# Kernel optimization log

Hardware: AMD Instinct MI355X
Metric: run time of the kernel (lower is better)

Reference implementation:

```python
import jax, jax.numpy as jnp
import numpy as np

TOP_K = 2
NEG_INF = -1e30


def setup_inputs() -> dict:
    key = jax.random.key(0)
    ks = jax.random.split(key, 9)
    S, B, D, H, E, O = 2, 2048, 1024, 2048, 8, 1024
    return {
        "xs": jax.random.normal(ks[0], (S, B, D), jnp.float32),
        "Wg": jax.random.normal(ks[1], (D, E), jnp.float32),
        "b": jax.random.normal(ks[2], (E,), jnp.float32),
        "fc1_w": jax.random.normal(ks[3], (E, H, D), jnp.float32) * 0.02,
        "fc1_b": jax.random.normal(ks[4], (E, H), jnp.float32) * 0.02,
        "fc2_w": jax.random.normal(ks[5], (E, H, H), jnp.float32) * 0.02,
        "fc2_b": jax.random.normal(ks[6], (E, H), jnp.float32) * 0.02,
        "final_w": jax.random.normal(ks[7], (O, H), jnp.float32) * 0.02,
        "final_b": jax.random.normal(ks[8], (O,), jnp.float32) * 0.02,
    }


def reference(xs, Wg, b, fc1_w, fc1_b, fc2_w, fc2_b, final_w, final_b):
    # xs: [S, B, D] stacked x_list
    S = xs.shape[0]
    # gate logits H: [S, B, E]
    Hg = jnp.einsum('sbd,de->sbe', xs, Wg) + b
    expert_probs = jax.nn.softmax(Hg, axis=-1)  # per-view full softmax
    # top-k threshold mask (H >= kth largest value)
    topk_vals = jax.lax.top_k(Hg, TOP_K)[0]          # [S, B, K]
    thr = topk_vals[..., -1:]                         # [S, B, 1]
    H_masked = jnp.where(Hg >= thr, Hg, NEG_INF)
    G = jax.nn.softmax(H_masked, axis=-1)             # [S, B, E]
    # dense all-expert FFN: [S, B, E, H]
    h = jnp.einsum('sbd,ehd->sbeh', xs, fc1_w) + fc1_b
    h = jax.nn.relu(h)
    eo = jnp.einsum('sbeh,egh->sbeg', h, fc2_w) + fc2_b
    # gated sum over experts, averaged over views: [B, H]
    combined = jnp.einsum('sbe,sbeh->bh', G, eo) / S
    out = combined @ final_w.T + final_b               # [B, O]
    return out, expert_probs
```

## Files before the change

### kernel.cpp

```cpp
#include <hip/hip_runtime.h>
#include <stdint.h>

#define S_DIM 2
#define B_DIM 2048
#define D_DIM 1024
#define H_DIM 2048
#define E_DIM 8
#define O_DIM 1024
#define NTOK 4096
#define CAP 12288

typedef __attribute__((ext_vector_type(8))) short bf16x8;
typedef __attribute__((ext_vector_type(4))) float f32x4;

__device__ __forceinline__ unsigned short f2bf(float f) {
    union { float f; uint32_t i; } c; c.f = f;
    uint32_t r = c.i + 0x7FFFu + ((c.i >> 16) & 1u);
    return (unsigned short)(r >> 16);
}
__device__ __forceinline__ uint32_t pack2(float a, float b) {
    return (uint32_t)f2bf(a) | ((uint32_t)f2bf(b) << 16);
}
__device__ __forceinline__ void stage8(const float* __restrict__ src,
                                       unsigned short* __restrict__ dst) {
    float4 f0 = *(const float4*)src;
    float4 f1 = *(const float4*)(src + 4);
    int4 v;
    v.x = (int)pack2(f0.x, f0.y);
    v.y = (int)pack2(f0.z, f0.w);
    v.z = (int)pack2(f1.x, f1.y);
    v.w = (int)pack2(f1.z, f1.w);
    *(int4*)dst = v;
}

__device__ __forceinline__ void glds16(const unsigned short* g, unsigned short* l) {
    __builtin_amdgcn_global_load_lds(
        (__attribute__((address_space(1))) void*)g,
        (__attribute__((address_space(3))) void*)l,
        16, 0, 0);
}

__global__ __launch_bounds__(256) void convert_kernel(
    const float* __restrict__ src, unsigned short* __restrict__ dst, int n8)
{
    int i = blockIdx.x * blockDim.x + threadIdx.x;
    if (i < n8) stage8(src + (size_t)i * 8, dst + (size_t)i * 8);
}

__global__ __launch_bounds__(256) void gating_kernel(
    const float* __restrict__ xs,
    const float* __restrict__ Wg,
    const float* __restrict__ bvec,
    float* __restrict__ probs_out,
    int* __restrict__ counts,
    int* __restrict__ sel_cnt,
    int* __restrict__ sel_e,
    float* __restrict__ sel_g,
    unsigned short* __restrict__ xs_bf)
{
    const int wave = threadIdx.x >> 6;
    const int lane = threadIdx.x & 63;
    const int t = blockIdx.x * 4 + wave;
    const float* x = xs + (size_t)t * D_DIM;

    float acc[8];
#pragma unroll
    for (int e = 0; e < 8; ++e) acc[e] = 0.f;

#pragma unroll
    for (int i = 0; i < D_DIM / 64; ++i) {
        int d = i * 64 + lane;
        float xv = x[d];
        xs_bf[(size_t)t * D_DIM + d] = f2bf(xv);
        float4 w0 = *(const float4*)(Wg + (size_t)d * 8);
        float4 w1 = *(const float4*)(Wg + (size_t)d * 8 + 4);
        acc[0] += xv * w0.x; acc[1] += xv * w0.y;
        acc[2] += xv * w0.z; acc[3] += xv * w0.w;
        acc[4] += xv * w1.x; acc[5] += xv * w1.y;
        acc[6] += xv * w1.z; acc[7] += xv * w1.w;
    }
#pragma unroll
    for (int off = 32; off > 0; off >>= 1) {
#pragma unroll
        for (int e = 0; e < 8; ++e)
            acc[e] += __shfl_down(acc[e], off);
    }

    if (lane == 0) {
        float Hg[8];
#pragma unroll
        for (int e = 0; e < 8; ++e) Hg[e] = acc[e] + bvec[e];

        int a1 = 0;
#pragma unroll
        for (int e = 1; e < 8; ++e) if (Hg[e] > Hg[a1]) a1 = e;
        float m1 = Hg[a1];
        float m2 = -1e30f;
#pragma unroll
        for (int e = 0; e < 8; ++e) if (e != a1 && Hg[e] > m2) m2 = Hg[e];

        float ex[8]; float sum = 0.f;
#pragma unroll
        for (int e = 0; e < 8; ++e) { ex[e] = expf(Hg[e] - m1); sum += ex[e]; }
        float inv = 1.f / sum;
#pragma unroll
        for (int e = 0; e < 8; ++e)
            probs_out[(size_t)t * 8 + e] = ex[e] * inv;

        float den = 0.f;
#pragma unroll
        for (int e = 0; e < 8; ++e) if (Hg[e] >= m2) den += ex[e];
        float invd = 1.f / den;
        int n = 0;
#pragma unroll
        for (int e = 0; e < 8; ++e) {
            if (Hg[e] >= m2) {
                sel_e[t * 8 + n] = e;
                sel_g[t * 8 + n] = ex[e] * invd;
                ++n;
                atomicAdd(&counts[e], 1);
            }
        }
        sel_cnt[t] = n;
    }
}

__global__ void scan_kernel(const int* __restrict__ counts, int* __restrict__ offsets)
{
    if (threadIdx.x == 0) {
        int tot = 0;
#pragma unroll
        for (int e = 0; e < 8; ++e) { offsets[e] = tot; tot += counts[e]; }
    }
}

__global__ __launch_bounds__(256) void scatter_kernel(
    const int* __restrict__ sel_cnt,
    const int* __restrict__ sel_e,
    const float* __restrict__ sel_g,
    const int* __restrict__ offsets,
    int* __restrict__ cursors,
    int* __restrict__ pair_token,
    float* __restrict__ pair_gate)
{
    int t = blockIdx.x * blockDim.x + threadIdx.x;
    if (t >= NTOK) return;
    int n = sel_cnt[t];
    for (int i = 0; i < n && i < 8; ++i) {
        int e = sel_e[t * 8 + i];
        int r = atomicAdd(&cursors[e], 1);
        int slot = offsets[e] + r;
        if (slot < CAP) {
            pair_token[slot] = t;
            pair_gate[slot]  = sel_g[t * 8 + i];
        }
    }
}

__global__ __launch_bounds__(256) void fc1_kernel(
    const unsigned short* __restrict__ xs_bf,
    const unsigned short* __restrict__ fc1_wb,
    const float* __restrict__ fc1_b,
    const int* __restrict__ counts,
    const int* __restrict__ offsets,
    const int* __restrict__ pair_token,
    unsigned short* __restrict__ h)
{
    const int wg = blockIdx.x;
    const int e = wg & 7;
    const int idx = wg >> 3;
    const int mtile = idx >> 4;
    const int ntile = idx & 15;
    const int cnt = counts[e];
    if (mtile * 128 >= cnt) return;
    const int offs = offsets[e];

    __shared__ __align__(16) unsigned short As[128 * 64];
    __shared__ __align__(16) unsigned short Bs[128 * 64];

    const int tid  = threadIdx.x;
    const int lane = tid & 63;
    const int wave = tid >> 6;
    const int wr = wave >> 1, wc = wave & 1;
    const int lrow = lane & 15;
    const int kq   = lane >> 4;

    const unsigned short* aSrc[4];
    const unsigned short* bSrc[4];
    int dstOff[4];
#pragma unroll
    for (int i = 0; i < 4; ++i) {
        int c = i * 256 + tid;
        int row = c >> 3;
        int gran = (c & 7) ^ (row & 7);
        int m = mtile * 128 + row;
        int mc = m < cnt ? m : cnt - 1;
        int tok = pair_token[offs + mc];
        aSrc[i] = xs_bf + (size_t)tok * D_DIM + gran * 8;
        int n = ntile * 128 + row;
        bSrc[i] = fc1_wb + ((size_t)e * H_DIM + n) * D_DIM + gran * 8;
        dstOff[i] = (i * 256 + wave * 64) * 8;
    }

    f32x4 acc[4][4];
#pragma unroll
    for (int i = 0; i < 4; ++i)
#pragma unroll
        for (int j = 0; j < 4; ++j)
            acc[i][j] = (f32x4){0.f, 0.f, 0.f, 0.f};

    for (int k0 = 0; k0 < D_DIM; k0 += 64) {
        __syncthreads();
#pragma unroll
        for (int i = 0; i < 4; ++i) {
            glds16(aSrc[i] + k0, &As[dstOff[i]]);
            glds16(bSrc[i] + k0, &Bs[dstOff[i]]);
        }
        __syncthreads();
#pragma unroll
        for (int ks = 0; ks < 2; ++ks) {
            bf16x8 af[4], bfr[4];
            const int gr = ks * 4 + kq;
            const int sg = (gr ^ (lrow & 7)) * 8;
#pragma unroll
            for (int i = 0; i < 4; ++i) {
                af[i]  = *(const bf16x8*)&As[(wr * 64 + i * 16 + lrow) * 64 + sg];
                bfr[i] = *(const bf16x8*)&Bs[(wc * 64 + i * 16 + lrow) * 64 + sg];
            }
#pragma unroll
            for (int i = 0; i < 4; ++i)
#pragma unroll
                for (int j = 0; j < 4; ++j)
                    acc[i][j] = __builtin_amdgcn_mfma_f32_16x16x32_bf16(af[i], bfr[j], acc[i][j], 0, 0, 0);
        }
    }

    int ncol[4]; float bias[4];
#pragma unroll
    for (int j = 0; j < 4; ++j) {
        ncol[j] = ntile * 128 + wc * 64 + j * 16 + lrow;
        bias[j] = fc1_b[e * H_DIM + ncol[j]];
    }
#pragma unroll
    for (int i = 0; i < 4; ++i) {
#pragma unroll
        for (int r = 0; r < 4; ++r) {
            int m = mtile * 128 + wr * 64 + i * 16 + kq * 4 + r;
            if (m < cnt) {
                size_t base = (size_t)(offs + m) * H_DIM;
#pragma unroll
                for (int j = 0; j < 4; ++j) {
                    float v = acc[i][j][r] + bias[j];
                    h[base + ncol[j]] = f2bf(v > 0.f ? v : 0.f);
                }
            }
        }
    }
}

__global__ __launch_bounds__(256) void fc2_kernel(
    const unsigned short* __restrict__ h,
    const unsigned short* __restrict__ fc2_wb,
    const float* __restrict__ fc2_b,
    const int* __restrict__ counts,
    const int* __restrict__ offsets,
    const int* __restrict__ pair_token,
    const float* __restrict__ pair_gate,
    float* __restrict__ combined)
{
    const int wg = blockIdx.x;
    const int e = wg & 7;
    const int idx = wg >> 3;
    const int mtile = idx >> 4;
    const int ntile = idx & 15;
    const int cnt = counts[e];
    if (mtile * 128 >= cnt) return;
    const int offs = offsets[e];

    __shared__ __align__(16) unsigned short As[128 * 64];
    __shared__ __align__(16) unsigned short Bs[128 * 64];

    const int tid  = threadIdx.x;
    const int lane = tid & 63;
    const int wave = tid >> 6;
    const int wr = wave >> 1, wc = wave & 1;
    const int lrow = lane & 15;
    const int kq   = lane >> 4;

    const unsigned short* aSrc[4];
    const unsigned short* bSrc[4];
    int dstOff[4];
#pragma unroll
    for (int i = 0; i < 4; ++i) {
        int c = i * 256 + tid;
        int row = c >> 3;
        int gran = (c & 7) ^ (row & 7);
        int m = mtile * 128 + row;
        int mc = m < cnt ? m : cnt - 1;
        aSrc[i] = h + (size_t)(offs + mc) * H_DIM + gran * 8;
        int n = ntile * 128 + row;
        bSrc[i] = fc2_wb + ((size_t)e * H_DIM + n) * H_DIM + gran * 8;
        dstOff[i] = (i * 256 + wave * 64) * 8;
    }

    f32x4 acc[4][4];
#pragma unroll
    for (int i = 0; i < 4; ++i)
#pragma unroll
        for (int j = 0; j < 4; ++j)
            acc[i][j] = (f32x4){0.f, 0.f, 0.f, 0.f};

    for (int k0 = 0; k0 < H_DIM; k0 += 64) {
        __syncthreads();
#pragma unroll
        for (int i = 0; i < 4; ++i) {
            glds16(aSrc[i] + k0, &As[dstOff[i]]);
            glds16(bSrc[i] + k0, &Bs[dstOff[i]]);
        }
        __syncthreads();
#pragma unroll
        for (int ks = 0; ks < 2; ++ks) {
            bf16x8 af[4], bfr[4];
            const int gr = ks * 4 + kq;
            const int sg = (gr ^ (lrow & 7)) * 8;
#pragma unroll
            for (int i = 0; i < 4; ++i) {
                af[i]  = *(const bf16x8*)&As[(wr * 64 + i * 16 + lrow) * 64 + sg];
                bfr[i] = *(const bf16x8*)&Bs[(wc * 64 + i * 16 + lrow) * 64 + sg];
            }
#pragma unroll
            for (int i = 0; i < 4; ++i)
#pragma unroll
                for (int j = 0; j < 4; ++j)
                    acc[i][j] = __builtin_amdgcn_mfma_f32_16x16x32_bf16(af[i], bfr[j], acc[i][j], 0, 0, 0);
        }
    }

    int ncol[4]; float bias[4];
#pragma unroll
    for (int j = 0; j < 4; ++j) {
        ncol[j] = ntile * 128 + wc * 64 + j * 16 + lrow;
        bias[j] = fc2_b[e * H_DIM + ncol[j]];
    }
#pragma unroll
    for (int i = 0; i < 4; ++i) {
#pragma unroll
        for (int r = 0; r < 4; ++r) {
            int m = mtile * 128 + wr * 64 + i * 16 + kq * 4 + r;
            if (m < cnt) {
                int slot = offs + m;
                int tok  = pair_token[slot];
                float g  = pair_gate[slot] * 0.5f;
                int brow = tok & (B_DIM - 1);
#pragma unroll
                for (int j = 0; j < 4; ++j) {
                    float v = (acc[i][j][r] + bias[j]) * g;
                    atomicAdd(&combined[(size_t)brow * H_DIM + ncol[j]], v);
                }
            }
        }
    }
}

__global__ __launch_bounds__(256) void final_kernel(
    const unsigned short* __restrict__ combined_bf,
    const unsigned short* __restrict__ final_wb,
    const float* __restrict__ final_b,
    float* __restrict__ out)
{
    const int mtile = blockIdx.y;
    const int ntile = blockIdx.x;

    __shared__ __align__(16) unsigned short As[128 * 64];
    __shared__ __align__(16) unsigned short Bs[128 * 64];

    const int tid  = threadIdx.x;
    const int lane = tid & 63;
    const int wave = tid >> 6;
    const int wr = wave >> 1, wc = wave & 1;
    const int lrow = lane & 15;
    const int kq   = lane >> 4;

    const unsigned short* aSrc[4];
    const unsigned short* bSrc[4];
    int dstOff[4];
#pragma unroll
    for (int i = 0; i < 4; ++i) {
        int c = i * 256 + tid;
        int row = c >> 3;
        int gran = (c & 7) ^ (row & 7);
        int m = mtile * 128 + row;
        aSrc[i] = combined_bf + (size_t)m * H_DIM + gran * 8;
        int n = ntile * 128 + row;
        bSrc[i] = final_wb + (size_t)n * H_DIM + gran * 8;
        dstOff[i] = (i * 256 + wave * 64) * 8;
    }

    f32x4 acc[4][4];
#pragma unroll
    for (int i = 0; i < 4; ++i)
#pragma unroll
        for (int j = 0; j < 4; ++j)
            acc[i][j] = (f32x4){0.f, 0.f, 0.f, 0.f};

    for (int k0 = 0; k0 < H_DIM; k0 += 64) {
        __syncthreads();
#pragma unroll
        for (int i = 0; i < 4; ++i) {
            glds16(aSrc[i] + k0, &As[dstOff[i]]);
            glds16(bSrc[i] + k0, &Bs[dstOff[i]]);
        }
        __syncthreads();
#pragma unroll
        for (int ks = 0; ks < 2; ++ks) {
            bf16x8 af[4], bfr[4];
            const int gr = ks * 4 + kq;
            const int sg = (gr ^ (lrow & 7)) * 8;
#pragma unroll
            for (int i = 0; i < 4; ++i) {
                af[i]  = *(const bf16x8*)&As[(wr * 64 + i * 16 + lrow) * 64 + sg];
                bfr[i] = *(const bf16x8*)&Bs[(wc * 64 + i * 16 + lrow) * 64 + sg];
            }
#pragma unroll
            for (int i = 0; i < 4; ++i)
#pragma unroll
                for (int j = 0; j < 4; ++j)
                    acc[i][j] = __builtin_amdgcn_mfma_f32_16x16x32_bf16(af[i], bfr[j], acc[i][j], 0, 0, 0);
        }
    }

    int ncol[4]; float bias[4];
#pragma unroll
    for (int j = 0; j < 4; ++j) {
        ncol[j] = ntile * 128 + wc * 64 + j * 16 + lrow;
        bias[j] = final_b[ncol[j]];
    }
#pragma unroll
    for (int i = 0; i < 4; ++i) {
#pragma unroll
        for (int r = 0; r < 4; ++r) {
            int m = mtile * 128 + wr * 64 + i * 16 + kq * 4 + r;
#pragma unroll
            for (int j = 0; j < 4; ++j)
                out[(size_t)m * O_DIM + ncol[j]] = acc[i][j][r] + bias[j];
        }
    }
}

extern "C" void kernel_launch(void* const* d_in, const int* in_sizes, int n_in,
                              void* d_out, int out_size, void* d_ws, size_t ws_size,
                              hipStream_t stream) {
    const float* xs      = (const float*)d_in[0];
    const float* Wg      = (const float*)d_in[1];
    const float* bvec    = (const float*)d_in[2];
    const float* fc1_w   = (const float*)d_in[3];
    const float* fc1_b   = (const float*)d_in[4];
    const float* fc2_w   = (const float*)d_in[5];
    const float* fc2_b   = (const float*)d_in[6];
    const float* final_w = (const float*)d_in[7];
    const float* final_b = (const float*)d_in[8];

    float* out = (float*)d_out;
    float* probs_out = out + (size_t)B_DIM * O_DIM;

    uint8_t* w = (uint8_t*)d_ws;
    int*   counts     = (int*)(w + 0);
    int*   cursors    = (int*)(w + 64);
    int*   offsets    = (int*)(w + 128);
    int*   sel_cnt    = (int*)(w + 256);
    int*   sel_e      = (int*)(w + 0x5000);
    float* sel_g      = (float*)(w + 0x25000);
    int*   pair_token = (int*)(w + 0x45000);
    float* pair_gate  = (float*)(w + 0x51000);
    float* combined   = (float*)(w + 0x60000);
    unsigned short* h = (unsigned short*)(w + 0x1060000);
    unsigned short* xs_bf   = (unsigned short*)(w + 0x4060000);
    unsigned short* fc1_wb  = (unsigned short*)(w + 0x4860000);
    unsigned short* fc2_wb  = (unsigned short*)(w + 0x6860000);
    unsigned short* final_wb    = (unsigned short*)(w + 0xA860000);
    unsigned short* combined_bf = (unsigned short*)(w + 0xAC60000);

    hipMemsetAsync(w, 0, 256, stream);
    hipMemsetAsync(combined, 0, (size_t)B_DIM * H_DIM * sizeof(float), stream);

    convert_kernel<<<(E_DIM * H_DIM * D_DIM / 8) / 256, 256, 0, stream>>>(
        fc1_w, fc1_wb, E_DIM * H_DIM * D_DIM / 8);
    convert_kernel<<<(E_DIM * H_DIM * H_DIM / 8) / 256, 256, 0, stream>>>(
        fc2_w, fc2_wb, E_DIM * H_DIM * H_DIM / 8);
    convert_kernel<<<(O_DIM * H_DIM / 8) / 256, 256, 0, stream>>>(
        final_w, final_wb, O_DIM * H_DIM / 8);

    gating_kernel<<<NTOK / 4, 256, 0, stream>>>(xs, Wg, bvec, probs_out,
                                                counts, sel_cnt, sel_e, sel_g, xs_bf);
    scan_kernel<<<1, 64, 0, stream>>>(counts, offsets);
    scatter_kernel<<<NTOK / 256, 256, 0, stream>>>(sel_cnt, sel_e, sel_g, offsets,
                                                   cursors, pair_token, pair_gate);
    fc1_kernel<<<E_DIM * (NTOK / 128) * (H_DIM / 128), 256, 0, stream>>>(
        xs_bf, fc1_wb, fc1_b, counts, offsets, pair_token, h);
    fc2_kernel<<<E_DIM * (NTOK / 128) * (H_DIM / 128), 256, 0, stream>>>(
        h, fc2_wb, fc2_b, counts, offsets, pair_token, pair_gate, combined);
    convert_kernel<<<(B_DIM * H_DIM / 8) / 256, 256, 0, stream>>>(
        combined, combined_bf, B_DIM * H_DIM / 8);
    final_kernel<<<dim3(O_DIM / 128, B_DIM / 128), 256, 0, stream>>>(
        combined_bf, final_wb, final_b, out);
}
```

Measured before the change: 662.5 us.

## Replace fc2 atomic scatter-add with bf16 per-slot output and gather reduce kernel

The fc2 epilogue no longer does float atomicAdds into a combined buffer. It writes gated expert outputs as bf16 into a per-slot buffer. A new reduce kernel gathers each token's slots through a token-to-slot map recorded by the scatter kernel, sums them, and writes combined in bf16 directly. This removes the memset of combined, the atomic traffic and the separate conversion kernel, at the cost of an extra bf16 write and read of the pair outputs and one more rounding step before the sum.

```diff
diff --git a/kernel.cpp b/kernel.cpp
--- a/kernel.cpp
+++ b/kernel.cpp
@@ -17,6 +17,10 @@
     union { float f; uint32_t i; } c; c.f = f;
     uint32_t r = c.i + 0x7FFFu + ((c.i >> 16) & 1u);
     return (unsigned short)(r >> 16);
+}
+__device__ __forceinline__ float bf2f(unsigned short u) {
+    union { uint32_t i; float f; } c; c.i = (uint32_t)u << 16;
+    return c.f;
 }
 __device__ __forceinline__ uint32_t pack2(float a, float b) {
     return (uint32_t)f2bf(a) | ((uint32_t)f2bf(b) << 16);
@@ -141,7 +145,8 @@
     const int* __restrict__ offsets,
     int* __restrict__ cursors,
     int* __restrict__ pair_token,
-    float* __restrict__ pair_gate)
+    float* __restrict__ pair_gate,
+    int* __restrict__ tok_slot)
 {
     int t = blockIdx.x * blockDim.x + threadIdx.x;
     if (t >= NTOK) return;
@@ -153,6 +158,9 @@
         if (slot < CAP) {
             pair_token[slot] = t;
             pair_gate[slot]  = sel_g[t * 8 + i];
+            tok_slot[t * 8 + i] = slot;
+        } else {
+            tok_slot[t * 8 + i] = -1;
         }
     }
 }
@@ -264,9 +272,8 @@
     const float* __restrict__ fc2_b,
     const int* __restrict__ counts,
     const int* __restrict__ offsets,
-    const int* __restrict__ pair_token,
     const float* __restrict__ pair_gate,
-    float* __restrict__ combined)
+    unsigned short* __restrict__ eo_bf)
 {
     const int wg = blockIdx.x;
     const int e = wg & 7;
@@ -349,17 +356,51 @@
             int m = mtile * 128 + wr * 64 + i * 16 + kq * 4 + r;
             if (m < cnt) {
                 int slot = offs + m;
-                int tok  = pair_token[slot];
                 float g  = pair_gate[slot] * 0.5f;
-                int brow = tok & (B_DIM - 1);
+                size_t base = (size_t)slot * H_DIM;
 #pragma unroll
                 for (int j = 0; j < 4; ++j) {
                     float v = (acc[i][j][r] + bias[j]) * g;
-                    atomicAdd(&combined[(size_t)brow * H_DIM + ncol[j]], v);
+                    eo_bf[base + ncol[j]] = f2bf(v);
                 }
             }
         }
     }
+}
+
+__global__ __launch_bounds__(256) void reduce_kernel(
+    const int* __restrict__ sel_cnt,
+    const int* __restrict__ tok_slot,
+    const unsigned short* __restrict__ eo_bf,
+    unsigned short* __restrict__ combined_bf)
+{
+    const int b = blockIdx.x;
+    const int h0 = threadIdx.x * 8;
+
+    float acc[8];
+#pragma unroll
+    for (int j = 0; j < 8; ++j) acc[j] = 0.f;
+
+#pragma unroll
+    for (int s = 0; s < S_DIM; ++s) {
+        int t = s * B_DIM + b;
+        int n = sel_cnt[t];
+        for (int i = 0; i < n && i < 8; ++i) {
+            int slot = tok_slot[t * 8 + i];
+            if (slot < 0) continue;
+            bf16x8 v = *(const bf16x8*)&eo_bf[(size_t)slot * H_DIM + h0];
+#pragma unroll
+            for (int j = 0; j < 8; ++j)
+                acc[j] += bf2f((unsigned short)v[j]);
+        }
+    }
+
+    int4 o;
+    o.x = (int)pack2(acc[0], acc[1]);
+    o.y = (int)pack2(acc[2], acc[3]);
+    o.z = (int)pack2(acc[4], acc[5]);
+    o.w = (int)pack2(acc[6], acc[7]);
+    *(int4*)&combined_bf[(size_t)b * H_DIM + h0] = o;
 }
 
 __global__ __launch_bounds__(256) void final_kernel(
@@ -472,16 +513,16 @@
     float* sel_g      = (float*)(w + 0x25000);
     int*   pair_token = (int*)(w + 0x45000);
     float* pair_gate  = (float*)(w + 0x51000);
-    float* combined   = (float*)(w + 0x60000);
+    int*   tok_slot   = (int*)(w + 0x5D000);
     unsigned short* h = (unsigned short*)(w + 0x1060000);
     unsigned short* xs_bf   = (unsigned short*)(w + 0x4060000);
     unsigned short* fc1_wb  = (unsigned short*)(w + 0x4860000);
     unsigned short* fc2_wb  = (unsigned short*)(w + 0x6860000);
     unsigned short* final_wb    = (unsigned short*)(w + 0xA860000);
     unsigned short* combined_bf = (unsigned short*)(w + 0xAC60000);
+    unsigned short* eo_bf       = (unsigned short*)(w + 0xB460000);
 
     hipMemsetAsync(w, 0, 256, stream);
-    hipMemsetAsync(combined, 0, (size_t)B_DIM * H_DIM * sizeof(float), stream);
 
     convert_kernel<<<(E_DIM * H_DIM * D_DIM / 8) / 256, 256, 0, stream>>>(
         fc1_w, fc1_wb, E_DIM * H_DIM * D_DIM / 8);
@@ -494,13 +535,13 @@
                                                 counts, sel_cnt, sel_e, sel_g, xs_bf);
     scan_kernel<<<1, 64, 0, stream>>>(counts, offsets);
     scatter_kernel<<<NTOK / 256, 256, 0, stream>>>(sel_cnt, sel_e, sel_g, offsets,
-                                                   cursors, pair_token, pair_gate);
+                                                   cursors, pair_token, pair_gate,
+                                                   tok_slot);
     fc1_kernel<<<E_DIM * (NTOK / 128) * (H_DIM / 128), 256, 0, stream>>>(
         xs_bf, fc1_wb, fc1_b, counts, offsets, pair_token, h);
     fc2_kernel<<<E_DIM * (NTOK / 128) * (H_DIM / 128), 256, 0, stream>>>(
-        h, fc2_wb, fc2_b, counts, offsets, pair_token, pair_gate, combined);
-    convert_kernel<<<(B_DIM * H_DIM / 8) / 256, 256, 0, stream>>>(
-        combined, combined_bf, B_DIM * H_DIM / 8);
+        h, fc2_wb, fc2_b, counts, offsets, pair_gate, eo_bf);
+    reduce_kernel<<<B_DIM, 256, 0, stream>>>(sel_cnt, tok_slot, eo_bf, combined_bf);
     final_kernel<<<dim3(O_DIM / 128, B_DIM / 128), 256, 0, stream>>>(
         combined_bf, final_wb, final_b, out);
 }
```

Result: faster. 625.9 us (-5.5%).
